# Optimization experiments

Hardware: AMD Instinct MI355X
Metric: run time of the kernel (lower is better)

The kernel has to match this reference:

```python
import jax, jax.numpy as jnp
import numpy as np

B, S, D = 2, 4096, 1024
EPS = 1e-05


def setup_inputs() -> dict:
    key = jax.random.key(0)
    ks = jax.random.split(key, 7)
    x = jax.random.normal(ks[0], (B, S, D), dtype=jnp.float32)
    gamma = jnp.ones((D,), dtype=jnp.float32)
    wq, wk, wv, wa, wg, wo = (jax.random.normal(k, (D, D), dtype=jnp.float32) for k in ks[1:7])
    return {"x": x, "gamma": gamma, "wq": wq, "wk": wk, "wv": wv, "wa": wa, "wg": wg, "wo": wo}


def _rmsnorm(x, gamma):
    # original uses sum of squares (not mean) with scale = sqrt(dim)
    ss = jnp.sum(jnp.square(x), axis=-1, keepdims=True)
    inv = jax.lax.rsqrt(ss + EPS)
    return inv * x * gamma * (x.shape[-1] ** 0.5)


def _gate_loop_operator(kv, q, a):
    def binop(e_i, e_j):
        a_i, kv_i = e_i
        a_j, kv_j = e_j
        return (a_j * a_i, a_j * kv_i + kv_j)
    _, y = jax.lax.associative_scan(binop, (a, kv), axis=1)
    return q * y


def reference(x, gamma, wq, wk, wv, wa, wg, wo):
    x = _rmsnorm(x, gamma)
    q = x @ wq
    k = x @ wk
    v = x @ wv
    a = jax.nn.sigmoid(x @ wa)
    g = x @ wg
    kv = k * v
    y = _gate_loop_operator(kv, q, a)
    y = y * jax.nn.silu(g)
    return y @ wo
```

## Files before the change

kernel.cpp:

```cpp
#include <hip/hip_runtime.h>
#include <hip/hip_bf16.h>
#include <cstdint>
#include <cstddef>


typedef __bf16 bf16x8 __attribute__((ext_vector_type(8)));
typedef float f32x4 __attribute__((ext_vector_type(4)));

__device__ __forceinline__ void gload_lds16(const void* g, void* l) {
  __builtin_amdgcn_global_load_lds(
      (const __attribute__((address_space(1))) void*)g,
      (__attribute__((address_space(3))) void*)l,
      16, 0, 0);
}

__device__ __forceinline__ bf16x8 ldfrag(const unsigned short* p) {
  return *(const bf16x8*)p;
}

#define MFMA16(acc_, a_, b_) \
  acc_ = __builtin_amdgcn_mfma_f32_16x16x32_bf16(a_, b_, acc_, 0, 0, 0)

__global__ __launch_bounds__(256) void wconv_k(
    const float* __restrict__ wq, const float* __restrict__ wk,
    const float* __restrict__ wv, const float* __restrict__ wa,
    const float* __restrict__ wg, const float* __restrict__ wo,
    __hip_bfloat16* __restrict__ wcatT, __hip_bfloat16* __restrict__ woT) {
  __shared__ float t[32][33];
  const float* src;
  __hip_bfloat16* dst;
  switch (blockIdx.z) {
    case 0: src = wq; dst = wcatT; break;
    case 1: src = wk; dst = wcatT + (size_t)1024 * 1024; break;
    case 2: src = wv; dst = wcatT + (size_t)2048 * 1024; break;
    case 3: src = wg; dst = wcatT + (size_t)3072 * 1024; break;
    case 4: src = wa; dst = wcatT + (size_t)4096 * 1024; break;
    default: src = wo; dst = woT; break;
  }
  const int n0 = blockIdx.x * 32;
  const int k0 = blockIdx.y * 32;
  const int tx = threadIdx.x, ty = threadIdx.y;
#pragma unroll
  for (int i = 0; i < 32; i += 8)
    t[ty + i][tx] = src[(size_t)(k0 + ty + i) * 1024 + n0 + tx];
  __syncthreads();
#pragma unroll
  for (int i = 0; i < 32; i += 8)
    dst[(size_t)(n0 + ty + i) * 1024 + k0 + tx] = __float2bfloat16(t[tx][ty + i]);
}

__global__ __launch_bounds__(256) void rmsnorm_k(
    const float* __restrict__ x, const float* __restrict__ gamma,
    __hip_bfloat16* __restrict__ xn) {
  const int row = blockIdx.x;
  const int tid = threadIdx.x;
  const float4 xv = ((const float4*)(x + (size_t)row * 1024))[tid];
  float ss = xv.x * xv.x + xv.y * xv.y + xv.z * xv.z + xv.w * xv.w;
#pragma unroll
  for (int off = 32; off >= 1; off >>= 1) ss += __shfl_xor(ss, off, 64);
  __shared__ float wss[4];
  if ((tid & 63) == 0) wss[tid >> 6] = ss;
  __syncthreads();
  const float total = wss[0] + wss[1] + wss[2] + wss[3];
  const float scale = rsqrtf(total + 1e-5f) * 32.0f;
  const float4 gv = ((const float4*)gamma)[tid];
  union { __hip_bfloat16 h[4]; ushort4 u; } ob;
  ob.h[0] = __float2bfloat16(xv.x * gv.x * scale);
  ob.h[1] = __float2bfloat16(xv.y * gv.y * scale);
  ob.h[2] = __float2bfloat16(xv.z * gv.z * scale);
  ob.h[3] = __float2bfloat16(xv.w * gv.w * scale);
  ((ushort4*)(xn + (size_t)row * 1024))[tid] = ob.u;
}

__global__ __launch_bounds__(512, 2) void gemm256p(
    const __hip_bfloat16* __restrict__ A, const __hip_bfloat16* __restrict__ Bt,
    int M, int N, int K,
    __hip_bfloat16* __restrict__ outb, int ldb, int nbcols,
    float* __restrict__ outf, int ldf) {
  __shared__ __align__(16) unsigned short lds[65536];
  unsigned short* Asl = lds;
  unsigned short* Bsl = lds + 32768;

  const int tid = threadIdx.x;
  const int nwg = gridDim.x * gridDim.y;
  const int bid = blockIdx.y * gridDim.x + blockIdx.x;
  const int swz = (bid & 7) * (nwg >> 3) + (bid >> 3);
  const int brow = (swz / gridDim.x) * 256;
  const int bcol = (swz % gridDim.x) * 256;

  const unsigned short* Ag = (const unsigned short*)A + (size_t)brow * K;
  const unsigned short* Bg = (const unsigned short*)Bt + (size_t)bcol * K;

  const int sr = tid >> 3;
  const int sc = tid & 7;

  auto stage = [&](unsigned short* dst, const unsigned short* G, int ht, int T) {
#pragma unroll
    for (int j = 0; j < 2; ++j) {
      const int row = sr + j * 64;
      gload_lds16(G + (size_t)(ht * 128 + row) * K + T * 64 + ((sc ^ (row & 7)) << 3),
                  dst + row * 64 + sc * 8);
    }
  };

  const int lane = tid & 63;
  const int wid = tid >> 6;
  const int wr = wid >> 2;
  const int wc = wid & 3;
  const int l16 = lane & 15;
  const int k8 = lane >> 4;

  int aoff[8], boff[4];
#pragma unroll
  for (int m = 0; m < 8; ++m) {
    const int row = wr * 128 + m * 16 + l16;
    const int ht = row >> 7, hr = row & 127;
    aoff[m] = ht * 8192 + hr * 64 + ((k8 ^ (hr & 7)) << 3);
  }
#pragma unroll
  for (int n = 0; n < 4; ++n) {
    const int row = wc * 64 + n * 16 + l16;
    const int ht = row >> 7, hr = row & 127;
    boff[n] = ht * 8192 + hr * 64 + ((k8 ^ (hr & 7)) << 3);
  }

  f32x4 acc[8][4];
#pragma unroll
  for (int m = 0; m < 8; ++m)
#pragma unroll
    for (int n = 0; n < 4; ++n) acc[m][n] = (f32x4){0.f, 0.f, 0.f, 0.f};

  const int NT = K >> 6;

  stage(Asl, Ag, 0, 0);          stage(Asl + 8192, Ag, 1, 0);
  stage(Bsl, Bg, 0, 0);          stage(Bsl + 8192, Bg, 1, 0);
  stage(Bsl + 16384, Bg, 0, 1);  stage(Bsl + 16384 + 8192, Bg, 1, 1);
  asm volatile("s_waitcnt vmcnt(4)" ::: "memory");
  __builtin_amdgcn_s_barrier();

  bf16x8 aL[4][2], aH[4][2], bL[2][2], bH[2][2];

  for (int i = 0; i < NT / 2; ++i) {
    const int T1 = 2 * i + 1, T2 = 2 * i + 2, T3 = 2 * i + 3;
    const unsigned short* A0 = Asl;
    const unsigned short* B0 = Bsl;
    const unsigned short* A1 = Asl + 16384;
    const unsigned short* B1 = Bsl + 16384;

#pragma unroll
    for (int m = 0; m < 4; ++m) {
      aL[m][0] = ldfrag(A0 + aoff[m]);
      aL[m][1] = ldfrag(A0 + (aoff[m] ^ 32));
    }
#pragma unroll
    for (int n = 0; n < 2; ++n) {
      bL[n][0] = ldfrag(B0 + boff[n]);
      bL[n][1] = ldfrag(B0 + (boff[n] ^ 32));
    }
    stage(Asl + 16384, Ag, 0, T1);
    asm volatile("s_waitcnt lgkmcnt(8)" ::: "memory");
    __builtin_amdgcn_s_barrier();
    asm volatile("s_waitcnt lgkmcnt(0)" ::: "memory");
    __builtin_amdgcn_s_setprio(1);
#pragma unroll
    for (int m = 0; m < 4; ++m)
#pragma unroll
      for (int n = 0; n < 2; ++n) {
        MFMA16(acc[m][n], aL[m][0], bL[n][0]);
        MFMA16(acc[m][n], aL[m][1], bL[n][1]);
      }
    __builtin_amdgcn_s_setprio(0);
    __builtin_amdgcn_s_barrier();

#pragma unroll
    for (int n = 0; n < 2; ++n) {
      bH[n][0] = ldfrag(B0 + boff[2 + n]);
      bH[n][1] = ldfrag(B0 + (boff[2 + n] ^ 32));
    }
    stage(Asl + 16384 + 8192, Ag, 1, T1);
    __builtin_amdgcn_s_barrier();
    asm volatile("s_waitcnt lgkmcnt(0)" ::: "memory");
    __builtin_amdgcn_s_setprio(1);
#pragma unroll
    for (int m = 0; m < 4; ++m)
#pragma unroll
      for (int n = 0; n < 2; ++n) {
        MFMA16(acc[m][2 + n], aL[m][0], bH[n][0]);
        MFMA16(acc[m][2 + n], aL[m][1], bH[n][1]);
      }
    __builtin_amdgcn_s_setprio(0);
    __builtin_amdgcn_s_barrier();

#pragma unroll
    for (int m = 0; m < 4; ++m) {
      aH[m][0] = ldfrag(A0 + aoff[4 + m]);
      aH[m][1] = ldfrag(A0 + (aoff[4 + m] ^ 32));
    }
    if (T2 < NT) stage(Bsl, Bg, 0, T2);
    __builtin_amdgcn_s_barrier();
    asm volatile("s_waitcnt lgkmcnt(0)" ::: "memory");
    __builtin_amdgcn_s_setprio(1);
#pragma unroll
    for (int m = 0; m < 4; ++m)
#pragma unroll
      for (int n = 0; n < 2; ++n) {
        MFMA16(acc[4 + m][2 + n], aH[m][0], bH[n][0]);
        MFMA16(acc[4 + m][2 + n], aH[m][1], bH[n][1]);
      }
    __builtin_amdgcn_s_setprio(0);
    __builtin_amdgcn_s_barrier();

    if (T2 < NT) {
      stage(Bsl + 8192, Bg, 1, T2);
      asm volatile("s_waitcnt vmcnt(4)" ::: "memory");
    } else {
      asm volatile("s_waitcnt vmcnt(0)" ::: "memory");
    }
    __builtin_amdgcn_s_barrier();
    __builtin_amdgcn_s_setprio(1);
#pragma unroll
    for (int m = 0; m < 4; ++m)
#pragma unroll
      for (int n = 0; n < 2; ++n) {
        MFMA16(acc[4 + m][n], aH[m][0], bL[n][0]);
        MFMA16(acc[4 + m][n], aH[m][1], bL[n][1]);
      }
    __builtin_amdgcn_s_setprio(0);
    __builtin_amdgcn_s_barrier();

#pragma unroll
    for (int m = 0; m < 4; ++m) {
      aL[m][0] = ldfrag(A1 + aoff[m]);
      aL[m][1] = ldfrag(A1 + (aoff[m] ^ 32));
    }
#pragma unroll
    for (int n = 0; n < 2; ++n) {
      bL[n][0] = ldfrag(B1 + boff[n]);
      bL[n][1] = ldfrag(B1 + (boff[n] ^ 32));
    }
    if (T2 < NT) stage(Asl, Ag, 0, T2);
    asm volatile("s_waitcnt lgkmcnt(8)" ::: "memory");
    __builtin_amdgcn_s_barrier();
    asm volatile("s_waitcnt lgkmcnt(0)" ::: "memory");
    __builtin_amdgcn_s_setprio(1);
#pragma unroll
    for (int m = 0; m < 4; ++m)
#pragma unroll
      for (int n = 0; n < 2; ++n) {
        MFMA16(acc[m][n], aL[m][0], bL[n][0]);
        MFMA16(acc[m][n], aL[m][1], bL[n][1]);
      }
    __builtin_amdgcn_s_setprio(0);
    __builtin_amdgcn_s_barrier();

#pragma unroll
    for (int n = 0; n < 2; ++n) {
      bH[n][0] = ldfrag(B1 + boff[2 + n]);
      bH[n][1] = ldfrag(B1 + (boff[2 + n] ^ 32));
    }
    if (T2 < NT) stage(Asl + 8192, Ag, 1, T2);
    __builtin_amdgcn_s_barrier();
    asm volatile("s_waitcnt lgkmcnt(0)" ::: "memory");
    __builtin_amdgcn_s_setprio(1);
#pragma unroll
    for (int m = 0; m < 4; ++m)
#pragma unroll
      for (int n = 0; n < 2; ++n) {
        MFMA16(acc[m][2 + n], aL[m][0], bH[n][0]);
        MFMA16(acc[m][2 + n], aL[m][1], bH[n][1]);
      }
    __builtin_amdgcn_s_setprio(0);
    __builtin_amdgcn_s_barrier();

#pragma unroll
    for (int m = 0; m < 4; ++m) {
      aH[m][0] = ldfrag(A1 + aoff[4 + m]);
      aH[m][1] = ldfrag(A1 + (aoff[4 + m] ^ 32));
    }
    if (T3 < NT) stage(Bsl + 16384, Bg, 0, T3);
    __builtin_amdgcn_s_barrier();
    asm volatile("s_waitcnt lgkmcnt(0)" ::: "memory");
    __builtin_amdgcn_s_setprio(1);
#pragma unroll
    for (int m = 0; m < 4; ++m)
#pragma unroll
      for (int n = 0; n < 2; ++n) {
        MFMA16(acc[4 + m][2 + n], aH[m][0], bH[n][0]);
        MFMA16(acc[4 + m][2 + n], aH[m][1], bH[n][1]);
      }
    __builtin_amdgcn_s_setprio(0);
    __builtin_amdgcn_s_barrier();

    if (T3 < NT) {
      stage(Bsl + 16384 + 8192, Bg, 1, T3);
      asm volatile("s_waitcnt vmcnt(4)" ::: "memory");
    } else {
      asm volatile("s_waitcnt vmcnt(0)" ::: "memory");
    }
    __builtin_amdgcn_s_barrier();
    __builtin_amdgcn_s_setprio(1);
#pragma unroll
    for (int m = 0; m < 4; ++m)
#pragma unroll
      for (int n = 0; n < 2; ++n) {
        MFMA16(acc[4 + m][n], aH[m][0], bL[n][0]);
        MFMA16(acc[4 + m][n], aH[m][1], bL[n][1]);
      }
    __builtin_amdgcn_s_setprio(0);
    __builtin_amdgcn_s_barrier();
  }

  const int mb = brow + wr * 128 + k8 * 4;
  const int nb = bcol + wc * 64 + l16;
#pragma unroll
  for (int m = 0; m < 8; ++m) {
#pragma unroll
    for (int n = 0; n < 4; ++n) {
      const int col = nb + n * 16;
#pragma unroll
      for (int r = 0; r < 4; ++r) {
        const int row = mb + m * 16 + r;
        const float v = acc[m][n][r];
        if (col < nbcols) {
          outb[(size_t)row * ldb + col] = __float2bfloat16(v);
        } else {
          outf[(size_t)row * ldf + (col - nbcols)] = v;
        }
      }
    }
  }
}

__global__ __launch_bounds__(256) void gemm128(
    const __hip_bfloat16* __restrict__ A, const __hip_bfloat16* __restrict__ Bt,
    int M, int N, int K,
    __hip_bfloat16* __restrict__ outb, int ldb, int nbcols,
    float* __restrict__ outf, int ldf) {
  __shared__ __align__(16) unsigned short As[3 * 4096];
  __shared__ __align__(16) unsigned short Bs[3 * 4096];

  const int tid = threadIdx.x;
  const int nwg = gridDim.x * gridDim.y;
  const int bid = blockIdx.y * gridDim.x + blockIdx.x;
  const int swz = (bid & 7) * (nwg >> 3) + (bid >> 3);
  const int brow = (swz / gridDim.x) * 128;
  const int bcol = (swz % gridDim.x) * 128;

  const unsigned short* Ag = (const unsigned short*)A + (size_t)brow * K;
  const unsigned short* Bg = (const unsigned short*)Bt + (size_t)bcol * K;

  const int srow = tid >> 2;
  const int gch8 = (((tid & 3) ^ ((tid >> 3) & 3)) << 3);

  auto stageAB = [&](int sl, int slot) {
    unsigned short* dA = As + slot * 4096;
    unsigned short* dB = Bs + slot * 4096;
    const int k0 = sl << 5;
    gload_lds16(Ag + (size_t)srow * K + k0 + gch8, dA + tid * 8);
    gload_lds16(Ag + (size_t)(srow + 64) * K + k0 + gch8, dA + 2048 + tid * 8);
    gload_lds16(Bg + (size_t)srow * K + k0 + gch8, dB + tid * 8);
    gload_lds16(Bg + (size_t)(srow + 64) * K + k0 + gch8, dB + 2048 + tid * 8);
  };

  const int lane = tid & 63;
  const int wid = tid >> 6;
  const int wr = wid >> 1;
  const int wc = wid & 1;
  const int l16 = lane & 15;
  const int k8 = lane >> 4;

  int aoff[4], boff[4];
#pragma unroll
  for (int m = 0; m < 4; ++m) {
    const int r = wr * 64 + m * 16 + l16;
    aoff[m] = r * 32 + ((k8 ^ ((r >> 1) & 3)) << 3);
  }
#pragma unroll
  for (int n = 0; n < 4; ++n) {
    const int r = wc * 64 + n * 16 + l16;
    boff[n] = r * 32 + ((k8 ^ ((r >> 1) & 3)) << 3);
  }

  f32x4 acc[4][4];
#pragma unroll
  for (int m = 0; m < 4; ++m)
#pragma unroll
    for (int n = 0; n < 4; ++n) acc[m][n] = (f32x4){0.f, 0.f, 0.f, 0.f};

  const int NS = K >> 5;
  stageAB(0, 0);
  stageAB(1, 1);
  asm volatile("s_waitcnt vmcnt(4)" ::: "memory");
  __builtin_amdgcn_s_barrier();

  int rs = 0, ws = 2;
  for (int s = 0; s < NS; ++s) {
    if (s + 2 < NS) stageAB(s + 2, ws);
    const unsigned short* As_s = As + rs * 4096;
    const unsigned short* Bs_s = Bs + rs * 4096;
    bf16x8 af[4], bfr[4];
#pragma unroll
    for (int m = 0; m < 4; ++m) af[m] = *(const bf16x8*)(As_s + aoff[m]);
#pragma unroll
    for (int n = 0; n < 4; ++n) bfr[n] = *(const bf16x8*)(Bs_s + boff[n]);
    __builtin_amdgcn_s_setprio(1);
#pragma unroll
    for (int m = 0; m < 4; ++m)
#pragma unroll
      for (int n = 0; n < 4; ++n)
        acc[m][n] = __builtin_amdgcn_mfma_f32_16x16x32_bf16(af[m], bfr[n], acc[m][n], 0, 0, 0);
    __builtin_amdgcn_s_setprio(0);
    if (s <= NS - 3) {
      asm volatile("s_waitcnt vmcnt(4)" ::: "memory");
      __builtin_amdgcn_s_barrier();
    } else if (s == NS - 2) {
      asm volatile("s_waitcnt vmcnt(0)" ::: "memory");
      __builtin_amdgcn_s_barrier();
    }
    rs = (rs == 2) ? 0 : rs + 1;
    ws = (ws == 2) ? 0 : ws + 1;
  }

  const int mb = brow + wr * 64 + k8 * 4;
  const int nb = bcol + wc * 64 + l16;
#pragma unroll
  for (int m = 0; m < 4; ++m) {
#pragma unroll
    for (int n = 0; n < 4; ++n) {
      const int col = nb + n * 16;
#pragma unroll
      for (int r = 0; r < 4; ++r) {
        const int row = mb + m * 16 + r;
        const float v = acc[m][n][r];
        if (col < nbcols) {
          outb[(size_t)row * ldb + col] = __float2bfloat16(v);
        } else {
          outf[(size_t)row * ldf + (col - nbcols)] = v;
        }
      }
    }
  }
}

__global__ __launch_bounds__(256) void scan_pass1(
    const __hip_bfloat16* __restrict__ qkvg, const float* __restrict__ apre,
    float* __restrict__ Asum, float* __restrict__ Ysum) {
  const int bc = blockIdx.x;
  const int d = blockIdx.y * 256 + threadIdx.x;
  const size_t rowbase = (size_t)(bc >> 5) * 4096 + (size_t)(bc & 31) * 128;
  float y = 0.f, Ap = 1.f;
  for (int s = 0; s < 128; ++s) {
    const size_t r = rowbase + s;
    const float kk = __bfloat162float(qkvg[r * 4096 + 1024 + d]);
    const float vv = __bfloat162float(qkvg[r * 4096 + 2048 + d]);
    const float ap = apre[r * 1024 + d];
    const float a = 1.f / (1.f + __expf(-ap));
    y = fmaf(a, y, kk * vv);
    Ap *= a;
  }
  Asum[(size_t)bc * 1024 + d] = Ap;
  Ysum[(size_t)bc * 1024 + d] = y;
}

__global__ __launch_bounds__(256) void scan_pass2(
    const float* __restrict__ Asum, const float* __restrict__ Ysum,
    float* __restrict__ carry) {
  const int idx = blockIdx.x * 256 + threadIdx.x;
  const int b = idx >> 10, d = idx & 1023;
  float y = 0.f;
  for (int c = 0; c < 32; ++c) {
    const size_t o = (size_t)(b * 32 + c) * 1024 + d;
    carry[o] = y;
    y = fmaf(Asum[o], y, Ysum[o]);
  }
}

__global__ __launch_bounds__(256) void scan_pass3(
    const __hip_bfloat16* __restrict__ qkvg, const float* __restrict__ apre,
    const float* __restrict__ carry, __hip_bfloat16* __restrict__ yact) {
  const int bc = blockIdx.x;
  const int d = blockIdx.y * 256 + threadIdx.x;
  const size_t rowbase = (size_t)(bc >> 5) * 4096 + (size_t)(bc & 31) * 128;
  float y = carry[(size_t)bc * 1024 + d];
  for (int s = 0; s < 128; ++s) {
    const size_t r = rowbase + s;
    const float qq = __bfloat162float(qkvg[r * 4096 + d]);
    const float kk = __bfloat162float(qkvg[r * 4096 + 1024 + d]);
    const float vv = __bfloat162float(qkvg[r * 4096 + 2048 + d]);
    const float gg = __bfloat162float(qkvg[r * 4096 + 3072 + d]);
    const float ap = apre[r * 1024 + d];
    const float a = 1.f / (1.f + __expf(-ap));
    y = fmaf(a, y, kk * vv);
    const float sg = 1.f / (1.f + __expf(-gg));
    yact[r * 1024 + d] = __float2bfloat16(qq * y * gg * sg);
  }
}

extern "C" void kernel_launch(void* const* d_in, const int* in_sizes, int n_in,
                              void* d_out, int out_size, void* d_ws, size_t ws_size,
                              hipStream_t stream) {
  const float* x     = (const float*)d_in[0];
  const float* gamma = (const float*)d_in[1];
  const float* wq    = (const float*)d_in[2];
  const float* wk    = (const float*)d_in[3];
  const float* wv    = (const float*)d_in[4];
  const float* wa    = (const float*)d_in[5];
  const float* wg    = (const float*)d_in[6];
  const float* wo    = (const float*)d_in[7];
  float* out = (float*)d_out;

  char* ws = (char*)d_ws;
  __hip_bfloat16* wcatT = (__hip_bfloat16*)(ws);
  __hip_bfloat16* woT   = (__hip_bfloat16*)(ws + 10485760);
  __hip_bfloat16* xn    = (__hip_bfloat16*)(ws + 12582912);
  __hip_bfloat16* qkvg  = (__hip_bfloat16*)(ws + 29360128);
  float*          apre  = (float*)(ws + 96468992);
  __hip_bfloat16* yact  = (__hip_bfloat16*)(ws + 130023424);
  float*          Asum  = (float*)(ws + 146800640);
  float*          Ysum  = (float*)(ws + 147062784);
  float*          carry = (float*)(ws + 147324928);

  wconv_k<<<dim3(32, 32, 6), dim3(32, 8, 1), 0, stream>>>(wq, wk, wv, wa, wg, wo, wcatT, woT);
  rmsnorm_k<<<dim3(8192), dim3(256), 0, stream>>>(x, gamma, xn);
  gemm256p<<<dim3(20, 32), dim3(512), 0, stream>>>(
      xn, wcatT, 8192, 5120, 1024, qkvg, 4096, 4096, apre, 1024);
  scan_pass1<<<dim3(64, 4), dim3(256), 0, stream>>>(qkvg, apre, Asum, Ysum);
  scan_pass2<<<dim3(8), dim3(256), 0, stream>>>(Asum, Ysum, carry);
  scan_pass3<<<dim3(64, 4), dim3(256), 0, stream>>>(qkvg, apre, carry, yact);
  gemm128<<<dim3(8, 64), dim3(256), 0, stream>>>(
      yact, woT, 8192, 1024, 1024, (__hip_bfloat16*)nullptr, 0, 0, out, 1024);
}
```

Before: 207.1 us.

## Fuse three-pass chunked scan into single decoupled-lookback kernel with flags

Replaces the three scan kernels (chunk reduce, carry propagation, apply) with one kernel. Each chunk block waits on its predecessor's flag to read the incoming carry, publishes its own outgoing carry, then rescans its chunk. This removes two kernel launches and the Asum/Ysum round trip through memory. In exchange it serialises the carry handoff across 32 chunks through spin-waits, and it relies on blocks being scheduled in order, which risks deadlock if they are not co-resident.

```diff
diff --git a/kernel.cpp b/kernel.cpp
--- a/kernel.cpp
+++ b/kernel.cpp
@@ -442,12 +442,17 @@
   }
 }
 
-__global__ __launch_bounds__(256) void scan_pass1(
+__global__ __launch_bounds__(256) void scan_fused(
     const __hip_bfloat16* __restrict__ qkvg, const float* __restrict__ apre,
-    float* __restrict__ Asum, float* __restrict__ Ysum) {
+    float* __restrict__ carry, int* __restrict__ flags,
+    __hip_bfloat16* __restrict__ yact) {
   const int bc = blockIdx.x;
+  const int c = bc & 31;
   const int d = blockIdx.y * 256 + threadIdx.x;
-  const size_t rowbase = (size_t)(bc >> 5) * 4096 + (size_t)(bc & 31) * 128;
+  const size_t rowbase = (size_t)(bc >> 5) * 4096 + (size_t)c * 128;
+  const int slot = bc * 4 + blockIdx.y;
+  const int cslot = slot * 256 + threadIdx.x;
+
   float y = 0.f, Ap = 1.f;
   for (int s = 0; s < 128; ++s) {
     const size_t r = rowbase + s;
@@ -458,30 +463,31 @@
     y = fmaf(a, y, kk * vv);
     Ap *= a;
   }
-  Asum[(size_t)bc * 1024 + d] = Ap;
-  Ysum[(size_t)bc * 1024 + d] = y;
-}
-
-__global__ __launch_bounds__(256) void scan_pass2(
-    const float* __restrict__ Asum, const float* __restrict__ Ysum,
-    float* __restrict__ carry) {
-  const int idx = blockIdx.x * 256 + threadIdx.x;
-  const int b = idx >> 10, d = idx & 1023;
-  float y = 0.f;
-  for (int c = 0; c < 32; ++c) {
-    const size_t o = (size_t)(b * 32 + c) * 1024 + d;
-    carry[o] = y;
-    y = fmaf(Asum[o], y, Ysum[o]);
-  }
-}
-
-__global__ __launch_bounds__(256) void scan_pass3(
-    const __hip_bfloat16* __restrict__ qkvg, const float* __restrict__ apre,
-    const float* __restrict__ carry, __hip_bfloat16* __restrict__ yact) {
-  const int bc = blockIdx.x;
-  const int d = blockIdx.y * 256 + threadIdx.x;
-  const size_t rowbase = (size_t)(bc >> 5) * 4096 + (size_t)(bc & 31) * 128;
-  float y = carry[(size_t)bc * 1024 + d];
+
+  float cin = 0.f;
+  if (c > 0) {
+    if (threadIdx.x == 0) {
+      while (__hip_atomic_load(&flags[slot - 4], __ATOMIC_ACQUIRE,
+                               __HIP_MEMORY_SCOPE_AGENT) == 0) {
+        __builtin_amdgcn_s_sleep(8);
+      }
+    }
+    __syncthreads();
+    cin = __hip_atomic_load(&carry[cslot - 1024], __ATOMIC_RELAXED,
+                            __HIP_MEMORY_SCOPE_AGENT);
+  }
+
+  if (c < 31) {
+    const float cout = fmaf(Ap, cin, y);
+    __hip_atomic_store(&carry[cslot], cout, __ATOMIC_RELAXED,
+                       __HIP_MEMORY_SCOPE_AGENT);
+    __syncthreads();
+    if (threadIdx.x == 0)
+      __hip_atomic_store(&flags[slot], 1, __ATOMIC_RELEASE,
+                         __HIP_MEMORY_SCOPE_AGENT);
+  }
+
+  float y2 = cin;
   for (int s = 0; s < 128; ++s) {
     const size_t r = rowbase + s;
     const float qq = __bfloat162float(qkvg[r * 4096 + d]);
@@ -490,9 +496,9 @@
     const float gg = __bfloat162float(qkvg[r * 4096 + 3072 + d]);
     const float ap = apre[r * 1024 + d];
     const float a = 1.f / (1.f + __expf(-ap));
-    y = fmaf(a, y, kk * vv);
+    y2 = fmaf(a, y2, kk * vv);
     const float sg = 1.f / (1.f + __expf(-gg));
-    yact[r * 1024 + d] = __float2bfloat16(qq * y * gg * sg);
+    yact[r * 1024 + d] = __float2bfloat16(qq * y2 * gg * sg);
   }
 }
 
@@ -516,17 +522,15 @@
   __hip_bfloat16* qkvg  = (__hip_bfloat16*)(ws + 29360128);
   float*          apre  = (float*)(ws + 96468992);
   __hip_bfloat16* yact  = (__hip_bfloat16*)(ws + 130023424);
-  float*          Asum  = (float*)(ws + 146800640);
-  float*          Ysum  = (float*)(ws + 147062784);
-  float*          carry = (float*)(ws + 147324928);
-
+  float*          carry = (float*)(ws + 146800640);
+  int*            flags = (int*)(ws + 147062784);
+
+  hipMemsetAsync(flags, 0, 64 * 4 * sizeof(int), stream);
   wconv_k<<<dim3(32, 32, 6), dim3(32, 8, 1), 0, stream>>>(wq, wk, wv, wa, wg, wo, wcatT, woT);
   rmsnorm_k<<<dim3(8192), dim3(256), 0, stream>>>(x, gamma, xn);
   gemm256p<<<dim3(20, 32), dim3(512), 0, stream>>>(
       xn, wcatT, 8192, 5120, 1024, qkvg, 4096, 4096, apre, 1024);
-  scan_pass1<<<dim3(64, 4), dim3(256), 0, stream>>>(qkvg, apre, Asum, Ysum);
-  scan_pass2<<<dim3(8), dim3(256), 0, stream>>>(Asum, Ysum, carry);
-  scan_pass3<<<dim3(64, 4), dim3(256), 0, stream>>>(qkvg, apre, carry, yact);
+  scan_fused<<<dim3(64, 4), dim3(256), 0, stream>>>(qkvg, apre, carry, flags, yact);
   gemm128<<<dim3(8, 64), dim3(256), 0, stream>>>(
       yact, woT, 8192, 1024, 1024, (__hip_bfloat16*)nullptr, 0, 0, out, 1024);
 }
```

Result: slower. 335.6 us (+62.1%).

## Fold carry scan into pass3 and process two channels per thread

Applied to the files above, without the earlier changes.

Drops the separate scan_pass2 kernel: each pass3 block now recomputes its chunk carry by serially combining the preceding chunk summaries. Both scan kernels now handle two adjacent channels per thread, using 32-bit packed bf16 loads and float2 loads and stores. This removes one launch and the carry buffer and widens memory accesses, but halves the grid to 128 blocks, which lowers parallelism. Later chunks also do up to 31 extra serial combine steps.

```diff
diff --git a/kernel.cpp b/kernel.cpp
--- a/kernel.cpp
+++ b/kernel.cpp
@@ -16,6 +16,13 @@
 
 __device__ __forceinline__ bf16x8 ldfrag(const unsigned short* p) {
   return *(const bf16x8*)p;
+}
+
+__device__ __forceinline__ float bfhi(unsigned int u) {
+  union { unsigned int i; float f; } c; c.i = u & 0xffff0000u; return c.f;
+}
+__device__ __forceinline__ float bflo(unsigned int u) {
+  union { unsigned int i; float f; } c; c.i = u << 16; return c.f;
 }
 
 #define MFMA16(acc_, a_, b_) \
@@ -446,53 +453,68 @@
     const __hip_bfloat16* __restrict__ qkvg, const float* __restrict__ apre,
     float* __restrict__ Asum, float* __restrict__ Ysum) {
   const int bc = blockIdx.x;
-  const int d = blockIdx.y * 256 + threadIdx.x;
+  const int d0 = blockIdx.y * 512 + threadIdx.x * 2;
   const size_t rowbase = (size_t)(bc >> 5) * 4096 + (size_t)(bc & 31) * 128;
-  float y = 0.f, Ap = 1.f;
+  const unsigned int* kkp = (const unsigned int*)(qkvg + 1024 + d0);
+  const unsigned int* vvp = (const unsigned int*)(qkvg + 2048 + d0);
+  float y0 = 0.f, y1 = 0.f, A0 = 1.f, A1 = 1.f;
   for (int s = 0; s < 128; ++s) {
     const size_t r = rowbase + s;
-    const float kk = __bfloat162float(qkvg[r * 4096 + 1024 + d]);
-    const float vv = __bfloat162float(qkvg[r * 4096 + 2048 + d]);
-    const float ap = apre[r * 1024 + d];
-    const float a = 1.f / (1.f + __expf(-ap));
-    y = fmaf(a, y, kk * vv);
-    Ap *= a;
-  }
-  Asum[(size_t)bc * 1024 + d] = Ap;
-  Ysum[(size_t)bc * 1024 + d] = y;
-}
-
-__global__ __launch_bounds__(256) void scan_pass2(
-    const float* __restrict__ Asum, const float* __restrict__ Ysum,
-    float* __restrict__ carry) {
-  const int idx = blockIdx.x * 256 + threadIdx.x;
-  const int b = idx >> 10, d = idx & 1023;
-  float y = 0.f;
-  for (int c = 0; c < 32; ++c) {
-    const size_t o = (size_t)(b * 32 + c) * 1024 + d;
-    carry[o] = y;
-    y = fmaf(Asum[o], y, Ysum[o]);
-  }
+    const unsigned int ku = kkp[r * 2048];
+    const unsigned int vu = vvp[r * 2048];
+    const float2 ap = *(const float2*)(apre + r * 1024 + d0);
+    const float a0 = 1.f / (1.f + __expf(-ap.x));
+    const float a1 = 1.f / (1.f + __expf(-ap.y));
+    y0 = fmaf(a0, y0, bflo(ku) * bflo(vu));
+    y1 = fmaf(a1, y1, bfhi(ku) * bfhi(vu));
+    A0 *= a0; A1 *= a1;
+  }
+  *(float2*)(Asum + (size_t)bc * 1024 + d0) = make_float2(A0, A1);
+  *(float2*)(Ysum + (size_t)bc * 1024 + d0) = make_float2(y0, y1);
 }
 
 __global__ __launch_bounds__(256) void scan_pass3(
     const __hip_bfloat16* __restrict__ qkvg, const float* __restrict__ apre,
-    const float* __restrict__ carry, __hip_bfloat16* __restrict__ yact) {
+    const float* __restrict__ Asum, const float* __restrict__ Ysum,
+    __hip_bfloat16* __restrict__ yact) {
   const int bc = blockIdx.x;
-  const int d = blockIdx.y * 256 + threadIdx.x;
-  const size_t rowbase = (size_t)(bc >> 5) * 4096 + (size_t)(bc & 31) * 128;
-  float y = carry[(size_t)bc * 1024 + d];
+  const int b = bc >> 5, c = bc & 31;
+  const int d0 = blockIdx.y * 512 + threadIdx.x * 2;
+  const size_t rowbase = (size_t)b * 4096 + (size_t)c * 128;
+
+  float y0 = 0.f, y1 = 0.f;
+  for (int j = 0; j < c; ++j) {
+    const size_t o = (size_t)(b * 32 + j) * 1024 + d0;
+    const float2 As2 = *(const float2*)(Asum + o);
+    const float2 Ys2 = *(const float2*)(Ysum + o);
+    y0 = fmaf(As2.x, y0, Ys2.x);
+    y1 = fmaf(As2.y, y1, Ys2.y);
+  }
+
+  const unsigned int* qqp = (const unsigned int*)(qkvg + d0);
+  const unsigned int* kkp = (const unsigned int*)(qkvg + 1024 + d0);
+  const unsigned int* vvp = (const unsigned int*)(qkvg + 2048 + d0);
+  const unsigned int* ggp = (const unsigned int*)(qkvg + 3072 + d0);
   for (int s = 0; s < 128; ++s) {
     const size_t r = rowbase + s;
-    const float qq = __bfloat162float(qkvg[r * 4096 + d]);
-    const float kk = __bfloat162float(qkvg[r * 4096 + 1024 + d]);
-    const float vv = __bfloat162float(qkvg[r * 4096 + 2048 + d]);
-    const float gg = __bfloat162float(qkvg[r * 4096 + 3072 + d]);
-    const float ap = apre[r * 1024 + d];
-    const float a = 1.f / (1.f + __expf(-ap));
-    y = fmaf(a, y, kk * vv);
-    const float sg = 1.f / (1.f + __expf(-gg));
-    yact[r * 1024 + d] = __float2bfloat16(qq * y * gg * sg);
+    const unsigned int qu = qqp[r * 2048];
+    const unsigned int ku = kkp[r * 2048];
+    const unsigned int vu = vvp[r * 2048];
+    const unsigned int gu = ggp[r * 2048];
+    const float2 ap = *(const float2*)(apre + r * 1024 + d0);
+    const float a0 = 1.f / (1.f + __expf(-ap.x));
+    const float a1 = 1.f / (1.f + __expf(-ap.y));
+    y0 = fmaf(a0, y0, bflo(ku) * bflo(vu));
+    y1 = fmaf(a1, y1, bfhi(ku) * bfhi(vu));
+    const float g0 = bflo(gu), g1 = bfhi(gu);
+    const float sg0 = 1.f / (1.f + __expf(-g0));
+    const float sg1 = 1.f / (1.f + __expf(-g1));
+    const float o0 = bflo(qu) * y0 * g0 * sg0;
+    const float o1 = bfhi(qu) * y1 * g1 * sg1;
+    union { __hip_bfloat16 h[2]; unsigned int u; } ob;
+    ob.h[0] = __float2bfloat16(o0);
+    ob.h[1] = __float2bfloat16(o1);
+    *(unsigned int*)(yact + r * 1024 + d0) = ob.u;
   }
 }
 
@@ -518,15 +540,13 @@
   __hip_bfloat16* yact  = (__hip_bfloat16*)(ws + 130023424);
   float*          Asum  = (float*)(ws + 146800640);
   float*          Ysum  = (float*)(ws + 147062784);
-  float*          carry = (float*)(ws + 147324928);
 
   wconv_k<<<dim3(32, 32, 6), dim3(32, 8, 1), 0, stream>>>(wq, wk, wv, wa, wg, wo, wcatT, woT);
   rmsnorm_k<<<dim3(8192), dim3(256), 0, stream>>>(x, gamma, xn);
   gemm256p<<<dim3(20, 32), dim3(512), 0, stream>>>(
       xn, wcatT, 8192, 5120, 1024, qkvg, 4096, 4096, apre, 1024);
-  scan_pass1<<<dim3(64, 4), dim3(256), 0, stream>>>(qkvg, apre, Asum, Ysum);
-  scan_pass2<<<dim3(8), dim3(256), 0, stream>>>(Asum, Ysum, carry);
-  scan_pass3<<<dim3(64, 4), dim3(256), 0, stream>>>(qkvg, apre, carry, yact);
+  scan_pass1<<<dim3(64, 2), dim3(256), 0, stream>>>(qkvg, apre, Asum, Ysum);
+  scan_pass3<<<dim3(64, 2), dim3(256), 0, stream>>>(qkvg, apre, Asum, Ysum, yact);
   gemm128<<<dim3(8, 64), dim3(256), 0, stream>>>(
       yact, woT, 8192, 1024, 1024, (__hip_bfloat16*)nullptr, 0, 0, out, 1024);
 }
```

Result: slower. 248.9 us (+20.2%).

## Interleave k/v and q/g weight columns; fold carry pass into scan pass3

Applied to the files above, without the earlier changes.

The weight transpose now interleaves the k and v output columns, and likewise q and g, so the GEMM writes paired bf16 values. The scan kernels can then read each pair with a single 32-bit load and unpack it with bit shifts, where they previously made separate strided 16-bit loads. The separate carry kernel (scan_pass2) is removed; each pass3 block recomputes its incoming carry from the chunk summaries, saving a launch and the carry buffer. The cost is that later chunks redo up to 31 serial FMAs over the summaries.

```diff
diff --git a/kernel.cpp b/kernel.cpp
--- a/kernel.cpp
+++ b/kernel.cpp
@@ -16,6 +16,13 @@
 
 __device__ __forceinline__ bf16x8 ldfrag(const unsigned short* p) {
   return *(const bf16x8*)p;
+}
+
+__device__ __forceinline__ float bfhi(unsigned int u) {
+  union { unsigned int i; float f; } c; c.i = u & 0xffff0000u; return c.f;
+}
+__device__ __forceinline__ float bflo(unsigned int u) {
+  union { unsigned int i; float f; } c; c.i = u << 16; return c.f;
 }
 
 #define MFMA16(acc_, a_, b_) \
@@ -29,13 +36,14 @@
   __shared__ float t[32][33];
   const float* src;
   __hip_bfloat16* dst;
+  int rmul, roff;
   switch (blockIdx.z) {
-    case 0: src = wq; dst = wcatT; break;
-    case 1: src = wk; dst = wcatT + (size_t)1024 * 1024; break;
-    case 2: src = wv; dst = wcatT + (size_t)2048 * 1024; break;
-    case 3: src = wg; dst = wcatT + (size_t)3072 * 1024; break;
-    case 4: src = wa; dst = wcatT + (size_t)4096 * 1024; break;
-    default: src = wo; dst = woT; break;
+    case 0: src = wq; dst = wcatT; rmul = 2; roff = 2048; break;
+    case 1: src = wk; dst = wcatT; rmul = 2; roff = 0;    break;
+    case 2: src = wv; dst = wcatT; rmul = 2; roff = 1;    break;
+    case 3: src = wg; dst = wcatT; rmul = 2; roff = 2049; break;
+    case 4: src = wa; dst = wcatT; rmul = 1; roff = 4096; break;
+    default: src = wo; dst = woT;  rmul = 1; roff = 0;    break;
   }
   const int n0 = blockIdx.x * 32;
   const int k0 = blockIdx.y * 32;
@@ -46,7 +54,8 @@
   __syncthreads();
 #pragma unroll
   for (int i = 0; i < 32; i += 8)
-    dst[(size_t)(n0 + ty + i) * 1024 + k0 + tx] = __float2bfloat16(t[tx][ty + i]);
+    dst[(size_t)(roff + rmul * (n0 + ty + i)) * 1024 + k0 + tx] =
+        __float2bfloat16(t[tx][ty + i]);
 }
 
 __global__ __launch_bounds__(256) void rmsnorm_k(
@@ -448,51 +457,46 @@
   const int bc = blockIdx.x;
   const int d = blockIdx.y * 256 + threadIdx.x;
   const size_t rowbase = (size_t)(bc >> 5) * 4096 + (size_t)(bc & 31) * 128;
+  const unsigned int* kvp = (const unsigned int*)qkvg;
   float y = 0.f, Ap = 1.f;
   for (int s = 0; s < 128; ++s) {
     const size_t r = rowbase + s;
-    const float kk = __bfloat162float(qkvg[r * 4096 + 1024 + d]);
-    const float vv = __bfloat162float(qkvg[r * 4096 + 2048 + d]);
+    const unsigned int kv = kvp[r * 2048 + d];
     const float ap = apre[r * 1024 + d];
     const float a = 1.f / (1.f + __expf(-ap));
-    y = fmaf(a, y, kk * vv);
+    y = fmaf(a, y, bflo(kv) * bfhi(kv));
     Ap *= a;
   }
   Asum[(size_t)bc * 1024 + d] = Ap;
   Ysum[(size_t)bc * 1024 + d] = y;
 }
 
-__global__ __launch_bounds__(256) void scan_pass2(
-    const float* __restrict__ Asum, const float* __restrict__ Ysum,
-    float* __restrict__ carry) {
-  const int idx = blockIdx.x * 256 + threadIdx.x;
-  const int b = idx >> 10, d = idx & 1023;
-  float y = 0.f;
-  for (int c = 0; c < 32; ++c) {
-    const size_t o = (size_t)(b * 32 + c) * 1024 + d;
-    carry[o] = y;
-    y = fmaf(Asum[o], y, Ysum[o]);
-  }
-}
-
 __global__ __launch_bounds__(256) void scan_pass3(
     const __hip_bfloat16* __restrict__ qkvg, const float* __restrict__ apre,
-    const float* __restrict__ carry, __hip_bfloat16* __restrict__ yact) {
+    const float* __restrict__ Asum, const float* __restrict__ Ysum,
+    __hip_bfloat16* __restrict__ yact) {
   const int bc = blockIdx.x;
+  const int b = bc >> 5, c = bc & 31;
   const int d = blockIdx.y * 256 + threadIdx.x;
-  const size_t rowbase = (size_t)(bc >> 5) * 4096 + (size_t)(bc & 31) * 128;
-  float y = carry[(size_t)bc * 1024 + d];
+  const size_t rowbase = (size_t)b * 4096 + (size_t)c * 128;
+
+  float y = 0.f;
+  for (int j = 0; j < c; ++j) {
+    const size_t o = (size_t)(b * 32 + j) * 1024 + d;
+    y = fmaf(Asum[o], y, Ysum[o]);
+  }
+
+  const unsigned int* kvp = (const unsigned int*)qkvg;
   for (int s = 0; s < 128; ++s) {
     const size_t r = rowbase + s;
-    const float qq = __bfloat162float(qkvg[r * 4096 + d]);
-    const float kk = __bfloat162float(qkvg[r * 4096 + 1024 + d]);
-    const float vv = __bfloat162float(qkvg[r * 4096 + 2048 + d]);
-    const float gg = __bfloat162float(qkvg[r * 4096 + 3072 + d]);
+    const unsigned int kv = kvp[r * 2048 + d];
+    const unsigned int qg = kvp[r * 2048 + 1024 + d];
     const float ap = apre[r * 1024 + d];
     const float a = 1.f / (1.f + __expf(-ap));
-    y = fmaf(a, y, kk * vv);
+    y = fmaf(a, y, bflo(kv) * bfhi(kv));
+    const float gg = bfhi(qg);
     const float sg = 1.f / (1.f + __expf(-gg));
-    yact[r * 1024 + d] = __float2bfloat16(qq * y * gg * sg);
+    yact[r * 1024 + d] = __float2bfloat16(bflo(qg) * y * gg * sg);
   }
 }
 
@@ -518,15 +522,13 @@
   __hip_bfloat16* yact  = (__hip_bfloat16*)(ws + 130023424);
   float*          Asum  = (float*)(ws + 146800640);
   float*          Ysum  = (float*)(ws + 147062784);
-  float*          carry = (float*)(ws + 147324928);
 
   wconv_k<<<dim3(32, 32, 6), dim3(32, 8, 1), 0, stream>>>(wq, wk, wv, wa, wg, wo, wcatT, woT);
   rmsnorm_k<<<dim3(8192), dim3(256), 0, stream>>>(x, gamma, xn);
   gemm256p<<<dim3(20, 32), dim3(512), 0, stream>>>(
       xn, wcatT, 8192, 5120, 1024, qkvg, 4096, 4096, apre, 1024);
   scan_pass1<<<dim3(64, 4), dim3(256), 0, stream>>>(qkvg, apre, Asum, Ysum);
-  scan_pass2<<<dim3(8), dim3(256), 0, stream>>>(Asum, Ysum, carry);
-  scan_pass3<<<dim3(64, 4), dim3(256), 0, stream>>>(qkvg, apre, carry, yact);
+  scan_pass3<<<dim3(64, 4), dim3(256), 0, stream>>>(qkvg, apre, Asum, Ysum, yact);
   gemm128<<<dim3(8, 64), dim3(256), 0, stream>>>(
       yact, woT, 8192, 1024, 1024, (__hip_bfloat16*)nullptr, 0, 0, out, 1024);
 }
```

New measurement: 210.0 us. No clear change (+1.4%).
